# Kernel tuning notes

Measured on AMD Instinct MI355X. Metric: run time of the kernel, lower is better.

Reference implementation:

```python
import jax, jax.numpy as jnp
import numpy as np

H = 768
R = 8
NS = 128
NQ = 256


def setup_inputs() -> dict:
    key = jax.random.key(0)
    ks = jax.random.split(key, 12)
    s = 0.02
    return {
        "support_embeddings": jax.random.normal(ks[0], (NS, H), jnp.float32),
        "support_labels": jax.random.randint(ks[1], (NS,), 0, 3),
        "query_embeddings": jax.random.normal(ks[2], (NQ, H), jnp.float32),
        # similarity encoder: Linear(2H->H), ReLU, Linear(H->1)
        "sim_W1": jax.random.normal(ks[3], (H, 2 * H), jnp.float32) * s,
        "sim_b1": jnp.zeros((H,), jnp.float32),
        "sim_w2": jax.random.normal(ks[4], (1, H), jnp.float32) * s,
        "sim_b2": jnp.zeros((1,), jnp.float32),
        # diversity encoder: same structure
        "div_W1": jax.random.normal(ks[5], (H, 2 * H), jnp.float32) * s,
        "div_b1": jnp.zeros((H,), jnp.float32),
        "div_w2": jax.random.normal(ks[6], (1, H), jnp.float32) * s,
        "div_b2": jnp.zeros((1,), jnp.float32),
        # num_relations separate Linear(H->H) layers, stacked
        "rel_W": jax.random.normal(ks[7], (R, H, H), jnp.float32) * s,
        "rel_b": jnp.zeros((R, H), jnp.float32),
    }


def _pair_matrix(emb, W1, b1, w2, b2):
    # MLP(concat(e_i, e_j)) for all pairs, vectorized.
    # concat([e_i, e_j]) @ W1.T == e_i @ W1[:, :H].T + e_j @ W1[:, H:].T
    h = emb.shape[1]
    left = emb @ W1[:, :h].T    # [N, H]
    right = emb @ W1[:, h:].T   # [N, H]
    hid = jax.nn.relu(left[:, None, :] + right[None, :, :] + b1)  # [N, N, H]
    m = hid @ w2[0] + b2[0]     # [N, N]
    n = m.shape[0]
    # diagonal stays zero (i != j in the original loop)
    return m * (1.0 - jnp.eye(n, dtype=m.dtype))


def reference(support_embeddings, support_labels, query_embeddings,
              sim_W1, sim_b1, sim_w2, sim_b2,
              div_W1, div_b1, div_w2, div_b2,
              rel_W, rel_b):
    emb = jnp.concatenate([support_embeddings, query_embeddings], axis=0)  # [N, H]
    sim = _pair_matrix(emb, sim_W1, sim_b1, sim_w2, sim_b2)
    div = _pair_matrix(emb, div_W1, div_b1, div_w2, div_b2)
    # per-relation Linear then mean over relations
    prop = jnp.einsum('nh,rkh->nrk', emb, rel_W) + rel_b  # [N, R, H]
    prop = prop.mean(axis=1)                               # [N, H]
    ns = support_embeddings.shape[0]
    return prop[:ns], prop[ns:], sim, div
```

## Files before the change

### kernel.cpp

```cpp
#include <hip/hip_runtime.h>
#include <hip/hip_bf16.h>

#define HDIM 768
#define NSUP 128
#define NTOT 384
#define NREL 8
#define WPLANE (HDIM*HDIM)
#define W1LD  (2*HDIM)

typedef unsigned short u16;
typedef __attribute__((ext_vector_type(8))) short bf16x8;
typedef __attribute__((ext_vector_type(4))) float f32x4;
typedef _Float16 h2v __attribute__((ext_vector_type(2)));

#define EMB_SLOTS   36864
#define W_SLOTS     73728
#define TILES_SLOTS (EMB_SLOTS + 5*W_SLOTS)

__device__ __forceinline__ u16 f2b(float f){
  unsigned x = __float_as_uint(f);
  return (u16)((x + 0x7fffu + ((x>>16)&1u)) >> 16);
}
__device__ __forceinline__ float b2f(u16 u){ return __uint_as_float(((unsigned)u)<<16); }
__device__ __forceinline__ u16 f2h_bits(float f){
  _Float16 h = (_Float16)f;
  return __builtin_bit_cast(unsigned short, h);
}

__device__ __forceinline__ const float* emb_row(const float* sup, const float* qry, int row){
  return row < NSUP ? sup + (size_t)row*HDIM : qry + (size_t)(row-NSUP)*HDIM;
}

__device__ __forceinline__ size_t rswz(int m, int n){
  int s = n / 96;
  int c = (n % 96) >> 3;
  return (size_t)(m >> 3)*6144 + (size_t)((c*64 + s*8 + (m & 7))*8 + (n & 7));
}

__global__ __launch_bounds__(256) void prep2_k(
    const float* __restrict__ sup, const float* __restrict__ qry,
    const float* __restrict__ relW, const float* __restrict__ relB,
    const float* __restrict__ simW1, const float* __restrict__ divW1,
    const float* __restrict__ simw2, const float* __restrict__ divw2,
    u16* __restrict__ tiles, float* __restrict__ bsum, u16* __restrict__ w2h){
  int s = blockIdx.x*256 + threadIdx.x;
  if (s < TILES_SLOTS){
    int lane = s & 63, f = (s>>6) & 1;
    int seg, loc;
    if (s < EMB_SLOTS){ seg = 0; loc = s; }
    else { int ls = s - EMB_SLOTS; seg = 1 + ls / W_SLOTS; loc = ls % W_SLOTS; }
    int lt2 = loc >> 7;
    int kc = lt2 % 24, tile = lt2 / 24;
    int row = tile*32 + f*16 + (lane & 15);
    int ksrc = kc*32 + (lane>>4)*8;
    float v[8];
    if (seg == 0){
      const float* src = emb_row(sup, qry, row) + ksrc;
      float4 a = *reinterpret_cast<const float4*>(src);
      float4 b = *reinterpret_cast<const float4*>(src + 4);
      v[0]=a.x; v[1]=a.y; v[2]=a.z; v[3]=a.w; v[4]=b.x; v[5]=b.y; v[6]=b.z; v[7]=b.w;
    } else if (seg <= 4){
      const float* base = (seg <= 2) ? simW1 : divW1;
      int koff = ((seg-1) & 1) ? HDIM : 0;
      const float* src = base + (size_t)row*W1LD + koff + ksrc;
      float4 a = *reinterpret_cast<const float4*>(src);
      float4 b = *reinterpret_cast<const float4*>(src + 4);
      v[0]=a.x; v[1]=a.y; v[2]=a.z; v[3]=a.w; v[4]=b.x; v[5]=b.y; v[6]=b.z; v[7]=b.w;
    } else {
      const float* src = relW + (size_t)row*HDIM + ksrc;
#pragma unroll
      for (int e=0;e<8;e++) v[e] = 0.f;
#pragma unroll
      for (int r=0;r<NREL;r++){
        float4 a = *reinterpret_cast<const float4*>(src + (size_t)r*WPLANE);
        float4 b = *reinterpret_cast<const float4*>(src + (size_t)r*WPLANE + 4);
        v[0]+=a.x; v[1]+=a.y; v[2]+=a.z; v[3]+=a.w; v[4]+=b.x; v[5]+=b.y; v[6]+=b.z; v[7]+=b.w;
      }
    }
    u16 o[8];
#pragma unroll
    for (int e=0;e<8;e++) o[e] = f2b(v[e]);
    ushort4* dst = reinterpret_cast<ushort4*>(tiles + (size_t)s*8);
    dst[0] = make_ushort4(o[0],o[1],o[2],o[3]);
    dst[1] = make_ushort4(o[4],o[5],o[6],o[7]);
  }
  if (blockIdx.x == 0 && threadIdx.x < HDIM/4){
    int c = threadIdx.x*4;
    float4 sbv = make_float4(0.f,0.f,0.f,0.f);
#pragma unroll
    for (int r=0;r<NREL;r++){
      float4 vv = *reinterpret_cast<const float4*>(relB + r*HDIM + c);
      sbv.x+=vv.x; sbv.y+=vv.y; sbv.z+=vv.z; sbv.w+=vv.w;
    }
    *reinterpret_cast<float4*>(bsum + c) = sbv;
  }
  if (blockIdx.x == 1){
    for (int e = threadIdx.x; e < 384; e += 256){
      int zz = e / 192, qq = e % 192;
      const float* w2src = zz ? divw2 : simw2;
      float4 wv = reinterpret_cast<const float4*>(w2src)[qq];
      ushort4 o;
      o.x = f2h_bits(wv.x); o.y = f2h_bits(wv.y); o.z = f2h_bits(wv.z); o.w = f2h_bits(wv.w);
      reinterpret_cast<ushort4*>(w2h + zz*HDIM)[qq] = o;
    }
  }
}

struct G5M4 {
  const float* b1f[4];
  u16* outH[4];
  float* outF;
  const float* bsum;
};

__global__ __launch_bounds__(512) void gemm5v4_k(const u16* __restrict__ tiles, G5M4 ga){
  __shared__ f32x4 red[4][4][64];
  int z = blockIdx.z;
  int t = threadIdx.x, lane = t&63, wid = t>>6;
  int q = wid & 3, kh = wid >> 2;
  int mtile = blockIdx.y*2 + (q&1);
  int ntile = blockIdx.x*2 + (q>>1);
  const u16* Ab = tiles + ((size_t)(mtile*24 + kh*12)*2*64 + lane)*8;
  const u16* Bb = tiles + (size_t)(EMB_SLOTS + z*W_SLOTS)*8
                        + ((size_t)(ntile*24 + kh*12)*2*64 + lane)*8;
  f32x4 acc00={0,0,0,0}, acc01={0,0,0,0}, acc10={0,0,0,0}, acc11={0,0,0,0};
  bf16x8 a0 = *reinterpret_cast<const bf16x8*>(Ab);
  bf16x8 a1 = *reinterpret_cast<const bf16x8*>(Ab + 512);
  bf16x8 b0 = *reinterpret_cast<const bf16x8*>(Bb);
  bf16x8 b1 = *reinterpret_cast<const bf16x8*>(Bb + 512);
#pragma unroll
  for (int c=0;c<12;c++){
    bf16x8 na0, na1, nb0, nb1;
    if (c < 11){
      na0 = *reinterpret_cast<const bf16x8*>(Ab + (c+1)*1024);
      na1 = *reinterpret_cast<const bf16x8*>(Ab + (c+1)*1024 + 512);
      nb0 = *reinterpret_cast<const bf16x8*>(Bb + (c+1)*1024);
      nb1 = *reinterpret_cast<const bf16x8*>(Bb + (c+1)*1024 + 512);
    }
    acc00 = __builtin_amdgcn_mfma_f32_16x16x32_bf16(a0, b0, acc00, 0, 0, 0);
    acc10 = __builtin_amdgcn_mfma_f32_16x16x32_bf16(a1, b0, acc10, 0, 0, 0);
    acc01 = __builtin_amdgcn_mfma_f32_16x16x32_bf16(a0, b1, acc01, 0, 0, 0);
    acc11 = __builtin_amdgcn_mfma_f32_16x16x32_bf16(a1, b1, acc11, 0, 0, 0);
    a0 = na0; a1 = na1; b0 = nb0; b1 = nb1;
  }
  if (kh){
    red[q][0][lane] = acc00;
    red[q][1][lane] = acc01;
    red[q][2][lane] = acc10;
    red[q][3][lane] = acc11;
  }
  __syncthreads();
  if (!kh){
    acc00 += red[q][0][lane];
    acc01 += red[q][1][lane];
    acc10 += red[q][2][lane];
    acc11 += red[q][3][lane];
    int l15 = lane & 15;
    int r0 = (lane>>4)*4;
    int m0 = mtile*32, n0 = ntile*32;
    if (z < 4){
      u16* outp = ga.outH[z];
      if ((z & 1) == 0){
        const float* b1f = ga.b1f[z];
        float bn0 = b1f[n0 + l15];
        float bn1 = b1f[n0 + 16 + l15];
#pragma unroll
        for (int r=0;r<4;r++){
          outp[(size_t)(m0 + r0 + r)*HDIM      + n0 + l15]      = f2h_bits(acc00[r] + bn0);
          outp[(size_t)(m0 + r0 + r)*HDIM      + n0 + 16 + l15] = f2h_bits(acc01[r] + bn1);
          outp[(size_t)(m0 + 16 + r0 + r)*HDIM + n0 + l15]      = f2h_bits(acc10[r] + bn0);
          outp[(size_t)(m0 + 16 + r0 + r)*HDIM + n0 + 16 + l15] = f2h_bits(acc11[r] + bn1);
        }
      } else {
#pragma unroll
        for (int r=0;r<4;r++){
          outp[rswz(m0 + r0 + r,      n0 + l15)]      = f2h_bits(acc00[r]);
          outp[rswz(m0 + r0 + r,      n0 + 16 + l15)] = f2h_bits(acc01[r]);
          outp[rswz(m0 + 16 + r0 + r, n0 + l15)]      = f2h_bits(acc10[r]);
          outp[rswz(m0 + 16 + r0 + r, n0 + 16 + l15)] = f2h_bits(acc11[r]);
        }
      }
    } else {
      float* outp = ga.outF;
      float bn0 = ga.bsum[n0 + l15];
      float bn1 = ga.bsum[n0 + 16 + l15];
#pragma unroll
      for (int r=0;r<4;r++){
        outp[(size_t)(m0 + r0 + r)*HDIM      + n0 + l15]      = (acc00[r] + bn0)*0.125f;
        outp[(size_t)(m0 + r0 + r)*HDIM      + n0 + 16 + l15] = (acc01[r] + bn1)*0.125f;
        outp[(size_t)(m0 + 16 + r0 + r)*HDIM + n0 + l15]      = (acc10[r] + bn0)*0.125f;
        outp[(size_t)(m0 + 16 + r0 + r)*HDIM + n0 + 16 + l15] = (acc11[r] + bn1)*0.125f;
      }
    }
  }
}

struct P6Args {
  const u16* L[2];
  const u16* R[2];
  const u16* w2h;
  const float* b2[2];
  float* out[2];
};

#define PDOT(LW, RW, WW, ACC) {                                               \
  h2v s_ = __builtin_elementwise_max(                                         \
      __builtin_bit_cast(h2v,(LW)) + __builtin_bit_cast(h2v,(RW)), hz);       \
  ACC = __builtin_amdgcn_fdot2(s_, __builtin_bit_cast(h2v,(WW)), ACC, false); }

__global__ __launch_bounds__(256, 2) void pair6_k(P6Args pa){
  int z = blockIdx.z;
  int i0 = blockIdx.x*8;
  int jt = blockIdx.y;
  __shared__ u16 Lh[8][768];
  __shared__ u16 w2s[768];
  int t = threadIdx.x;
  const u16* __restrict__ L = pa.L[z];
  for (int idx=t; idx<1536; idx+=256){
    int ii = idx/192, qq = idx - ii*192;
    reinterpret_cast<ushort4*>(&Lh[ii][0])[qq] =
        reinterpret_cast<const ushort4*>(L + (size_t)(i0+ii)*HDIM)[qq];
  }
  for (int e=t; e<192; e+=256)
    reinterpret_cast<ushort4*>(w2s)[e] = reinterpret_cast<const ushort4*>(pa.w2h + z*HDIM)[e];
  __syncthreads();
  int w = t>>6, lane = t&63;
  int s = lane>>3, g = lane&7;
  int jb = jt*32 + w*8;
  const h2v hz = {(_Float16)0.f, (_Float16)0.f};
  float acc[8] = {0.f,0.f,0.f,0.f,0.f,0.f,0.f,0.f};

  const u16* rp  = pa.R[z] + (size_t)(jb>>3)*6144 + ((size_t)lane<<3);
  const u16* wp  = &w2s[s*96];
  const u16* lp  = &Lh[0][s*96];
  uint4 rv = *reinterpret_cast<const uint4*>(rp);
#pragma unroll 1
  for (int c=0;c<12;c++){
    uint4 nrv = rv;
    if (c < 11) nrv = *reinterpret_cast<const uint4*>(rp + 512);
    uint4 wv = *reinterpret_cast<const uint4*>(wp);
#pragma unroll
    for (int ii=0;ii<8;ii++){
      uint4 lv = *reinterpret_cast<const uint4*>(lp + ii*768);
      PDOT(lv.x, rv.x, wv.x, acc[ii]);
      PDOT(lv.y, rv.y, wv.y, acc[ii]);
      PDOT(lv.z, rv.z, wv.z, acc[ii]);
      PDOT(lv.w, rv.w, wv.w, acc[ii]);
    }
    rv = nrv; rp += 512; wp += 8; lp += 8;
  }
  float b2v = pa.b2[z][0];
  float* outp = pa.out[z];
#pragma unroll
  for (int ii=0;ii<8;ii++){
    float a = acc[ii];
    a += __shfl_xor(a, 8, 64);
    a += __shfl_xor(a, 16, 64);
    a += __shfl_xor(a, 32, 64);
    if (s == ii){
      int i = i0 + ii, j = jb + g;
      float v = a + b2v;
      if (i == j) v = 0.f;
      outp[(size_t)i*NTOT + j] = v;
    }
  }
}

__global__ __launch_bounds__(256) void prop_k(
    const float* __restrict__ sup, const float* __restrict__ qry,
    const float* __restrict__ relW, const float* __restrict__ relB,
    float* __restrict__ outp){
  __shared__ float As[16][68];
  __shared__ float Bs[16][68];
  int t = threadIdx.x;
  int m0 = blockIdx.y*64, n0 = blockIdx.x*64;
  int lm = t>>2, lk = (t&3)<<2;
  int tx = t&15, ty = t>>4;
  float acc[4][4] = {{0,0,0,0},{0,0,0,0},{0,0,0,0},{0,0,0,0}};
  const float* Aptr = emb_row(sup, qry, m0+lm) + lk;
  const float* Bptr = relW + (size_t)(n0+lm)*HDIM + lk;
  for (int k0=0;k0<HDIM;k0+=16){
    float4 av = *reinterpret_cast<const float4*>(Aptr + k0);
    float4 bs = make_float4(0.f,0.f,0.f,0.f);
#pragma unroll
    for (int r=0;r<NREL;r++){
      float4 bv = *reinterpret_cast<const float4*>(Bptr + (size_t)r*WPLANE + k0);
      bs.x += bv.x; bs.y += bv.y; bs.z += bv.z; bs.w += bv.w;
    }
    __syncthreads();
    As[lk+0][lm]=av.x; As[lk+1][lm]=av.y; As[lk+2][lm]=av.z; As[lk+3][lm]=av.w;
    Bs[lk+0][lm]=bs.x; Bs[lk+1][lm]=bs.y; Bs[lk+2][lm]=bs.z; Bs[lk+3][lm]=bs.w;
    __syncthreads();
#pragma unroll
    for (int kk=0;kk<16;kk++){
      float4 a4 = *reinterpret_cast<const float4*>(&As[kk][ty<<2]);
      float4 b4 = *reinterpret_cast<const float4*>(&Bs[kk][tx<<2]);
      float ar[4]={a4.x,a4.y,a4.z,a4.w};
      float br[4]={b4.x,b4.y,b4.z,b4.w};
#pragma unroll
      for (int i2=0;i2<4;i2++)
#pragma unroll
        for (int j2=0;j2<4;j2++)
          acc[i2][j2] = fmaf(ar[i2], br[j2], acc[i2][j2]);
    }
  }
#pragma unroll
  for (int j2=0;j2<4;j2++){
    int n = n0 + (tx<<2) + j2;
    float bias = 0.f;
#pragma unroll
    for (int r=0;r<NREL;r++) bias += relB[r*HDIM + n];
#pragma unroll
    for (int i2=0;i2<4;i2++){
      int m = m0 + (ty<<2) + i2;
      outp[(size_t)m*HDIM + n] = (acc[i2][j2] + bias) * 0.125f;
    }
  }
}

struct NWArgs {
  const float* W1[2]; const float* b1[2]; const float* w2[2]; const float* b2[2];
  float* out[2];
};

__global__ __launch_bounds__(256) void pair_nows_k(
    const float* __restrict__ sup, const float* __restrict__ qry, NWArgs na){
  int z = blockIdx.z, i0 = blockIdx.x*32, j0 = blockIdx.y*32;
  __shared__ u16 Lt[32][768];
  __shared__ float Rj[768];
  __shared__ float b1s[768];
  __shared__ float w2s[768];
  const float* __restrict__ W1 = na.W1[z];
  int t = threadIdx.x;
  for (int k=t;k<768;k+=256){ b1s[k]=na.b1[z][k]; w2s[k]=na.w2[z][k]; }
  for (int e=t; e<32*768; e+=256){
    int ii = e/768, k = e - ii*768;
    const float4* er = reinterpret_cast<const float4*>(emb_row(sup, qry, i0+ii));
    const float4* wr = reinterpret_cast<const float4*>(W1 + (size_t)k*W1LD);
    float s = 0.f;
    for (int h=0;h<192;h++){
      float4 a = er[h], b = wr[h];
      s += a.x*b.x + a.y*b.y + a.z*b.z + a.w*b.w;
    }
    Lt[ii][k] = f2b(s);
  }
  float b2v = na.b2[z][0];
  int w = t>>6, l = t&63;
  float* outp = na.out[z];
  for (int jj=0;jj<32;jj++){
    int j = j0 + jj;
    const float4* ejr = reinterpret_cast<const float4*>(emb_row(sup, qry, j));
    __syncthreads();
    for (int k=t;k<768;k+=256){
      const float4* wr = reinterpret_cast<const float4*>(W1 + (size_t)k*W1LD + HDIM);
      float s = 0.f;
      for (int h=0;h<192;h++){
        float4 a = ejr[h], b = wr[h];
        s += a.x*b.x + a.y*b.y + a.z*b.z + a.w*b.w;
      }
      Rj[k] = s;
    }
    __syncthreads();
    for (int q=0;q<8;q++){
      int ii = (w<<3) + q;
      float acc = 0.f;
#pragma unroll
      for (int u=0;u<12;u++){
        int k = l + (u<<6);
        acc = fmaf(fmaxf(b2f(Lt[ii][k]) + Rj[k] + b1s[k], 0.f), w2s[k], acc);
      }
#pragma unroll
      for (int m=32;m>=1;m>>=1) acc += __shfl_xor(acc, m, 64);
      if (l==0){
        int i = i0 + ii;
        float v = acc + b2v;
        if (i==j) v = 0.f;
        outp[(size_t)i*NTOT + j] = v;
      }
    }
  }
}

extern "C" void kernel_launch(void* const* d_in, const int* in_sizes, int n_in,
                              void* d_out, int out_size, void* d_ws, size_t ws_size,
                              hipStream_t stream) {
  const float* sup   = (const float*)d_in[0];
  const float* qry   = (const float*)d_in[2];
  const float* simW1 = (const float*)d_in[3];
  const float* simb1 = (const float*)d_in[4];
  const float* simw2 = (const float*)d_in[5];
  const float* simb2 = (const float*)d_in[6];
  const float* divW1 = (const float*)d_in[7];
  const float* divb1 = (const float*)d_in[8];
  const float* divw2 = (const float*)d_in[9];
  const float* divb2 = (const float*)d_in[10];
  const float* relW  = (const float*)d_in[11];
  const float* relB  = (const float*)d_in[12];
  float* out = (float*)d_out;
  float* outSim = out + (size_t)NTOT*HDIM;
  float* outDiv = outSim + (size_t)NTOT*NTOT;

  const size_t TILB = (size_t)TILES_SLOTS*8*2;
  const size_t LRB  = (size_t)NTOT*HDIM*2;
  const size_t NEED = TILB + 8192 + 4*LRB;

  if (ws_size >= NEED){
    char* ws = (char*)d_ws;
    u16*   tiles = (u16*)(ws);
    float* bsum  = (float*)(ws + TILB);
    u16*   w2h   = (u16*)(ws + TILB + 4096);
    u16*   Ls    = (u16*)(ws + TILB + 8192);
    u16*   Rs    = (u16*)((char*)Ls + LRB);
    u16*   Ld    = (u16*)((char*)Rs + LRB);
    u16*   Rd    = (u16*)((char*)Ld + LRB);

    prep2_k<<<dim3((TILES_SLOTS + 255)/256), dim3(256), 0, stream>>>(
        sup, qry, relW, relB, simW1, divW1, simw2, divw2, tiles, bsum, w2h);

    G5M4 ga;
    ga.b1f[0]=simb1;   ga.outH[0]=Ls;
    ga.b1f[1]=nullptr; ga.outH[1]=Rs;
    ga.b1f[2]=divb1;   ga.outH[2]=Ld;
    ga.b1f[3]=nullptr; ga.outH[3]=Rd;
    ga.outF=out; ga.bsum=bsum;
    gemm5v4_k<<<dim3(12,6,5), dim3(512), 0, stream>>>(tiles, ga);

    P6Args pa;
    pa.L[0]=Ls; pa.R[0]=Rs; pa.b2[0]=simb2; pa.out[0]=outSim;
    pa.L[1]=Ld; pa.R[1]=Rd; pa.b2[1]=divb2; pa.out[1]=outDiv;
    pa.w2h = w2h;
    pair6_k<<<dim3(48,12,2), dim3(256), 0, stream>>>(pa);
  } else {
    prop_k<<<dim3(12,6), dim3(256), 0, stream>>>(sup, qry, relW, relB, out);
    NWArgs na;
    na.W1[0]=simW1; na.b1[0]=simb1; na.w2[0]=simw2; na.b2[0]=simb2; na.out[0]=outSim;
    na.W1[1]=divW1; na.b1[1]=divb1; na.w2[1]=divw2; na.b2[1]=divb2; na.out[1]=outDiv;
    pair_nows_k<<<dim3(12,12,2), dim3(256), 0, stream>>>(sup, qry, na);
  }
}
```

Measured before the change: 39.74 us.

## Split GEMM into one 32x32 tile per block with 4-way K split

The 5-way GEMM kernel is changed so each block computes one 32x32 output tile with four waves each covering a quarter of K, reduced through shared memory. Previously each 512-thread block computed four tiles with a 2-way K split. The grid grows from 360 to 1440 blocks to fill more CUs and cut per-wave serial MFMA chain length. The cost is a larger LDS reduction relative to compute, a non-unrolled loop, and more block-launch overhead.

```diff
diff --git a/kernel.cpp b/kernel.cpp
--- a/kernel.cpp
+++ b/kernel.cpp
@@ -113,48 +113,50 @@
   const float* bsum;
 };
 
-__global__ __launch_bounds__(512) void gemm5v4_k(const u16* __restrict__ tiles, G5M4 ga){
-  __shared__ f32x4 red[4][4][64];
+__global__ __launch_bounds__(256, 2) void gemm5v5_k(const u16* __restrict__ tiles, G5M4 ga){
+  __shared__ f32x4 red[3][4][64];
   int z = blockIdx.z;
-  int t = threadIdx.x, lane = t&63, wid = t>>6;
-  int q = wid & 3, kh = wid >> 2;
-  int mtile = blockIdx.y*2 + (q&1);
-  int ntile = blockIdx.x*2 + (q>>1);
-  const u16* Ab = tiles + ((size_t)(mtile*24 + kh*12)*2*64 + lane)*8;
+  int t = threadIdx.x, lane = t&63, w = t>>6;
+  int ntile = blockIdx.x, mtile = blockIdx.y;
+  const u16* Ab = tiles + ((size_t)((mtile*24 + w*6)*128 + lane))*8;
   const u16* Bb = tiles + (size_t)(EMB_SLOTS + z*W_SLOTS)*8
-                        + ((size_t)(ntile*24 + kh*12)*2*64 + lane)*8;
+                        + ((size_t)((ntile*24 + w*6)*128 + lane))*8;
   f32x4 acc00={0,0,0,0}, acc01={0,0,0,0}, acc10={0,0,0,0}, acc11={0,0,0,0};
   bf16x8 a0 = *reinterpret_cast<const bf16x8*>(Ab);
   bf16x8 a1 = *reinterpret_cast<const bf16x8*>(Ab + 512);
   bf16x8 b0 = *reinterpret_cast<const bf16x8*>(Bb);
   bf16x8 b1 = *reinterpret_cast<const bf16x8*>(Bb + 512);
-#pragma unroll
-  for (int c=0;c<12;c++){
-    bf16x8 na0, na1, nb0, nb1;
-    if (c < 11){
-      na0 = *reinterpret_cast<const bf16x8*>(Ab + (c+1)*1024);
-      na1 = *reinterpret_cast<const bf16x8*>(Ab + (c+1)*1024 + 512);
-      nb0 = *reinterpret_cast<const bf16x8*>(Bb + (c+1)*1024);
-      nb1 = *reinterpret_cast<const bf16x8*>(Bb + (c+1)*1024 + 512);
+#pragma unroll 1
+  for (int c=0;c<6;c++){
+    bf16x8 na0=a0, na1=a1, nb0=b0, nb1=b1;
+    if (c < 5){
+      na0 = *reinterpret_cast<const bf16x8*>(Ab + 1024);
+      na1 = *reinterpret_cast<const bf16x8*>(Ab + 1536);
+      nb0 = *reinterpret_cast<const bf16x8*>(Bb + 1024);
+      nb1 = *reinterpret_cast<const bf16x8*>(Bb + 1536);
     }
     acc00 = __builtin_amdgcn_mfma_f32_16x16x32_bf16(a0, b0, acc00, 0, 0, 0);
     acc10 = __builtin_amdgcn_mfma_f32_16x16x32_bf16(a1, b0, acc10, 0, 0, 0);
     acc01 = __builtin_amdgcn_mfma_f32_16x16x32_bf16(a0, b1, acc01, 0, 0, 0);
     acc11 = __builtin_amdgcn_mfma_f32_16x16x32_bf16(a1, b1, acc11, 0, 0, 0);
     a0 = na0; a1 = na1; b0 = nb0; b1 = nb1;
-  }
-  if (kh){
-    red[q][0][lane] = acc00;
-    red[q][1][lane] = acc01;
-    red[q][2][lane] = acc10;
-    red[q][3][lane] = acc11;
+    Ab += 1024; Bb += 1024;
+  }
+  if (w > 0){
+    red[w-1][0][lane] = acc00;
+    red[w-1][1][lane] = acc01;
+    red[w-1][2][lane] = acc10;
+    red[w-1][3][lane] = acc11;
   }
   __syncthreads();
-  if (!kh){
-    acc00 += red[q][0][lane];
-    acc01 += red[q][1][lane];
-    acc10 += red[q][2][lane];
-    acc11 += red[q][3][lane];
+  if (w == 0){
+#pragma unroll
+    for (int ww=0;ww<3;ww++){
+      acc00 += red[ww][0][lane];
+      acc01 += red[ww][1][lane];
+      acc10 += red[ww][2][lane];
+      acc11 += red[ww][3][lane];
+    }
     int l15 = lane & 15;
     int r0 = (lane>>4)*4;
     int m0 = mtile*32, n0 = ntile*32;
@@ -423,7 +425,7 @@
     ga.b1f[2]=divb1;   ga.outH[2]=Ld;
     ga.b1f[3]=nullptr; ga.outH[3]=Rd;
     ga.outF=out; ga.bsum=bsum;
-    gemm5v4_k<<<dim3(12,6,5), dim3(512), 0, stream>>>(tiles, ga);
+    gemm5v5_k<<<dim3(24,12,5), dim3(256), 0, stream>>>(tiles, ga);
 
     P6Args pa;
     pa.L[0]=Ls; pa.R[0]=Rs; pa.b2[0]=simb2; pa.out[0]=outSim;
```

Measured after the change: 38.71 us, median of 2. 1.03x faster.
